# Kernel optimization log

Measured on AMD Instinct MI355X. Metric: run time of the kernel, lower is better.

## Reference

```python
import jax, jax.numpy as jnp
import numpy as np

B, T, C = 4, 2048, 1024
H = 16
D = C // H  # head_dim = 64


def setup_inputs() -> dict:
    key = jax.random.key(0)
    ks = jax.random.split(key, 9)
    s = 1.0 / np.sqrt(C)
    return {
        "x": jax.random.normal(ks[0], (B, T, C), dtype=jnp.float32),
        "Wk": jax.random.uniform(ks[1], (C, C), jnp.float32, -s, s),
        "bk": jax.random.uniform(ks[2], (C,), jnp.float32, -s, s),
        "Wq": jax.random.uniform(ks[3], (C, C), jnp.float32, -s, s),
        "bq": jax.random.uniform(ks[4], (C,), jnp.float32, -s, s),
        "Wv": jax.random.uniform(ks[5], (C, C), jnp.float32, -s, s),
        "bv": jax.random.uniform(ks[6], (C,), jnp.float32, -s, s),
        "Wp": jax.random.uniform(ks[7], (C, C), jnp.float32, -s, s),
        "bp": jax.random.uniform(ks[8], (C,), jnp.float32, -s, s),
    }


def reference(x, Wk, bk, Wq, bq, Wv, bv, Wp, bp):
    # projections -> (B, H, T, D)
    def split_heads(y):
        return y.reshape(B, T, H, D).transpose(0, 2, 1, 3)

    k = split_heads(x @ Wk.T + bk)
    q = split_heads(x @ Wq.T + bq)
    v = split_heads(x @ Wv.T + bv)

    att = jnp.einsum("bhtd,bhsd->bhts", q, k) / np.sqrt(D).astype(np.float32)
    causal = jnp.tril(jnp.ones((T, T), dtype=bool))
    att = jnp.where(causal, att, -jnp.inf)
    att = jax.nn.softmax(att, axis=-1)

    y = jnp.einsum("bhts,bhsd->bhtd", att, v)  # (B,H,T,D)
    y = y.transpose(0, 2, 1, 3).reshape(B, T, C)
    return y @ Wp.T + bp
```

## Files before the change

kernel.cpp:

```cpp
#include <hip/hip_runtime.h>
#include <hip/hip_bf16.h>

typedef unsigned short u16;
typedef unsigned int u32;
typedef short short8 __attribute__((ext_vector_type(8)));
typedef short short4v __attribute__((ext_vector_type(4)));
typedef float f32x4 __attribute__((ext_vector_type(4)));
typedef unsigned int u32x4 __attribute__((ext_vector_type(4)));

#define MFMA16(a, b, c) __builtin_amdgcn_mfma_f32_16x16x32_bf16((a), (b), (c), 0, 0, 0)

constexpr int kB = 4, kT = 2048, kC = 1024, kH = 16, kD = 64;
constexpr int kBT = kB * kT;
constexpr long kQKV = (long)kB * kH * kT * kD;
constexpr float kSC = 0.125f * 1.4426950408889634f;

__device__ inline u16 f2bf(float f) {
    __hip_bfloat16 h = __float2bfloat16(f);
    return *reinterpret_cast<u16*>(&h);
}
__device__ inline u32 pkbf_trunc(float lo, float hi) {
    return __builtin_amdgcn_perm(__builtin_bit_cast(u32, hi),
                                 __builtin_bit_cast(u32, lo), 0x07060302u);
}
__device__ inline u32 pkbf_rne(float lo, float hi) {
    return ((u32)f2bf(hi) << 16) | (u32)f2bf(lo);
}

__device__ inline void cp16(const u16* g, u16* l) {
    __builtin_amdgcn_global_load_lds(
        (const __attribute__((address_space(1))) unsigned int*)g,
        (__attribute__((address_space(3))) unsigned int*)l, 16, 0, 0);
}

__global__ __launch_bounds__(256) void cast_kernel(
    const float* __restrict__ x,  const float* __restrict__ Wk,
    const float* __restrict__ Wq, const float* __restrict__ Wv,
    const float* __restrict__ Wp,
    u16* __restrict__ xb, u16* __restrict__ wkb, u16* __restrict__ wqb,
    u16* __restrict__ wvb, u16* __restrict__ wpb)
{
    const long id = (long)blockIdx.x * 256 + threadIdx.x;
    const float* src;
    u16* dst;
    long off;
    if (id < 2097152) {
        src = x; dst = xb; off = id;
    } else {
        const long w = (id - 2097152) >> 18;
        off = (id - 2097152) & 262143;
        src = (w == 0) ? Wk : (w == 1) ? Wq : (w == 2) ? Wv : Wp;
        dst = (w == 0) ? wkb : (w == 1) ? wqb : (w == 2) ? wvb : wpb;
    }
    f32x4 v = *(const f32x4*)&src[off * 4];
    short4v s = {(short)f2bf(v[0]), (short)f2bf(v[1]),
                 (short)f2bf(v[2]), (short)f2bf(v[3])};
    *(short4v*)&dst[off * 4] = s;
}


__global__ __launch_bounds__(512, 4) void qkv_gemm_bf16(
    const u16* __restrict__ xb, const u16* __restrict__ wall,
    const float* __restrict__ bk, const float* __restrict__ bq,
    const float* __restrict__ bv,
    u16* __restrict__ kw, u16* __restrict__ qw, u16* __restrict__ vw)
{
    __shared__ __align__(16) u16 A2[2][128 * 64];
    __shared__ __align__(16) u16 B2[2][128 * 64];

    const int tid = threadIdx.x;
    const int lane = tid & 63;
    const int wid = tid >> 6;
    const int l15 = lane & 15;
    const int quad = lane >> 4;
    const int wr = wid & 1;
    const int wc = wid >> 1;
    const int m0 = blockIdx.x * 128;
    const int n0c = blockIdx.y * 128;

    f32x4 zero = {0.f, 0.f, 0.f, 0.f};
    f32x4 acc[4][2];
#pragma unroll
    for (int i = 0; i < 4; ++i)
#pragma unroll
        for (int j = 0; j < 2; ++j) acc[i][j] = zero;

    const u16* aS[2]; const u16* bS[2];
    int sD[2];
#pragma unroll
    for (int q = 0; q < 2; ++q) {
        const int slot = q * 512 + tid;
        const int row = slot >> 3, ch = slot & 7;
        aS[q] = xb + (long)(m0 + row) * kC + ((ch ^ (row & 7)) * 8);
        bS[q] = wall + (long)(n0c + row) * kC + ((ch ^ (row & 7)) * 8);
        sD[q] = row * 64 + ch * 8;
    }

    auto stage = [&](int buf, int t) {
        const long ko = (long)t * 64;
#pragma unroll
        for (int q = 0; q < 2; ++q) {
            cp16(aS[q] + ko, &A2[buf][sD[q]]);
            cp16(bS[q] + ko, &B2[buf][sD[q]]);
        }
    };

    int aOff[4][2], bOff[2][2];
#pragma unroll
    for (int i = 0; i < 4; ++i) {
        const int row = wr * 64 + i * 16 + l15;
#pragma unroll
        for (int k2 = 0; k2 < 2; ++k2)
            aOff[i][k2] = row * 64 + (((k2 * 4 + quad) ^ (row & 7)) * 8);
    }
#pragma unroll
    for (int j = 0; j < 2; ++j) {
        const int row = wc * 32 + j * 16 + l15;
#pragma unroll
        for (int k2 = 0; k2 < 2; ++k2)
            bOff[j][k2] = row * 64 + (((k2 * 4 + quad) ^ (row & 7)) * 8);
    }

    stage(0, 0);
    stage(1, 1);
    __syncthreads();

    for (int t = 0; t < 16; ++t) {
        const int c = t & 1;
        const u16* Ab = A2[c];
        const u16* Bb = B2[c];

        short8 am[4][2], bn[2][2];
#pragma unroll
        for (int i = 0; i < 4; ++i)
#pragma unroll
            for (int k2 = 0; k2 < 2; ++k2)
                am[i][k2] = *(const short8*)&Ab[aOff[i][k2]];
#pragma unroll
        for (int j = 0; j < 2; ++j)
#pragma unroll
            for (int k2 = 0; k2 < 2; ++k2)
                bn[j][k2] = *(const short8*)&Bb[bOff[j][k2]];

        __builtin_amdgcn_s_setprio(1);
#pragma unroll
        for (int i = 0; i < 4; ++i)
#pragma unroll
            for (int j = 0; j < 2; ++j) {
                acc[i][j] = MFMA16(am[i][0], bn[j][0], acc[i][j]);
                acc[i][j] = MFMA16(am[i][1], bn[j][1], acc[i][j]);
            }
        __builtin_amdgcn_s_setprio(0);

        if (t + 1 < 16) {
            __syncthreads();
            if (t + 2 < 16) stage(c, t + 2);
        }
    }

    const int z = (n0c >> 10);
    const float scale = (z == 1) ? kSC : 1.0f;
    const float* bias = (z == 0) ? bk : (z == 1) ? bq : bv;
#pragma unroll
    for (int j = 0; j < 2; ++j) {
        const int n = n0c + wc * 32 + j * 16 + l15;
        const int np = n & 1023;
        const float bias_f = bias[np];
        const int h = np >> 6, d = np & 63;
#pragma unroll
        for (int i = 0; i < 4; ++i) {
#pragma unroll
            for (int r = 0; r < 4; ++r) {
                const int m = m0 + wr * 64 + i * 16 + quad * 4 + r;
                const int b = m >> 11, tt = m & 2047;
                const float v = (acc[i][j][r] + bias_f) * scale;
                const int bh = b * kH + h;
                if (z == 2) {
                    vw[((long)bh * kD + d) * kT + tt] = f2bf(v);
                } else {
                    u16* dst = (z == 0) ? kw : qw;
                    dst[((long)bh * kT + tt) * kD + d] = f2bf(v);
                }
            }
        }
    }
}

__global__ __launch_bounds__(256) void qkv_gemm_kernel(
    const float* __restrict__ x,
    const float* __restrict__ Wk, const float* __restrict__ bk,
    const float* __restrict__ Wq, const float* __restrict__ bq,
    const float* __restrict__ Wv, const float* __restrict__ bv,
    u16* __restrict__ kw, u16* __restrict__ qw, u16* __restrict__ vw)
{
    __shared__ u16 As[128 * 32];
    __shared__ u16 Bs[128 * 32];
    const int tid = threadIdx.x;
    const int lane = tid & 63;
    const int wid = tid >> 6;
    const int l15 = lane & 15;
    const int quad = lane >> 4;
    const int m0 = blockIdx.x * 128;
    const int n0 = blockIdx.y * 128;
    const int z = blockIdx.z;

    const float* W = (z == 0) ? Wk : (z == 1) ? Wq : Wv;
    const float* bias = (z == 0) ? bk : (z == 1) ? bq : bv;

    f32x4 zero = {0.f, 0.f, 0.f, 0.f};
    f32x4 acc[4][4];
#pragma unroll
    for (int i = 0; i < 4; ++i)
#pragma unroll
        for (int j = 0; j < 4; ++j) acc[i][j] = zero;

    const int wm = (wid & 1) * 64;
    const int wn = (wid >> 1) * 64;
    const int row4 = tid >> 3;
    const int col4 = (tid & 7) * 4;

    for (int k0 = 0; k0 < kC; k0 += 32) {
#pragma unroll
        for (int p = 0; p < 4; ++p) {
            const int r = p * 32 + row4;
            f32x4 xa = *(const f32x4*)&x[(long)(m0 + r) * kC + k0 + col4];
            f32x4 wa = *(const f32x4*)&W[(long)(n0 + r) * kC + k0 + col4];
            short4v xs = {(short)f2bf(xa[0]), (short)f2bf(xa[1]),
                          (short)f2bf(xa[2]), (short)f2bf(xa[3])};
            short4v wsv = {(short)f2bf(wa[0]), (short)f2bf(wa[1]),
                           (short)f2bf(wa[2]), (short)f2bf(wa[3])};
            *(short4v*)&As[r * 32 + col4] = xs;
            *(short4v*)&Bs[r * 32 + col4] = wsv;
        }
        __syncthreads();
        short8 af[4], bfr[4];
#pragma unroll
        for (int mt = 0; mt < 4; ++mt)
            af[mt] = *(const short8*)&As[(wm + mt * 16 + l15) * 32 + quad * 8];
#pragma unroll
        for (int nt = 0; nt < 4; ++nt)
            bfr[nt] = *(const short8*)&Bs[(wn + nt * 16 + l15) * 32 + quad * 8];
#pragma unroll
        for (int mt = 0; mt < 4; ++mt)
#pragma unroll
            for (int nt = 0; nt < 4; ++nt)
                acc[mt][nt] = MFMA16(af[mt], bfr[nt], acc[mt][nt]);
        __syncthreads();
    }

    const float scale = (z == 1) ? kSC : 1.0f;
#pragma unroll
    for (int nt = 0; nt < 4; ++nt) {
        const int n = n0 + wn + nt * 16 + l15;
        const float bias_f = bias[n];
        const int h = n >> 6, d = n & 63;
#pragma unroll
        for (int mt = 0; mt < 4; ++mt) {
#pragma unroll
            for (int r = 0; r < 4; ++r) {
                const int m = m0 + wm + mt * 16 + quad * 4 + r;
                const int b = m >> 11, t = m & 2047;
                const float v = (acc[mt][nt][r] + bias_f) * scale;
                const int bh = b * kH + h;
                if (z == 2) {
                    vw[((long)bh * kD + d) * kT + t] = f2bf(v);
                } else {
                    u16* dst = (z == 0) ? kw : qw;
                    dst[((long)bh * kT + t) * kD + d] = f2bf(v);
                }
            }
        }
    }
}

__global__ __launch_bounds__(256, 4) void attn_kernel(
    const u16* qw, const u16* kw, const u16* vw, u16* ow)
{
    __shared__ u16 Ks[2][64 * 64];
    __shared__ u16 VT[2][64 * 64];

    const int tid = threadIdx.x;
    const int lane = tid & 63;
    const int wid = tid >> 6;
    const int l15 = lane & 15;
    const int quad = lane >> 4;
    const int id = blockIdx.x;
    const int bh = id & 63;
    constexpr int pperm[16] = {15, 14, 13, 12, 0, 1, 2, 3,
                               11, 10, 9, 8, 4, 5, 6, 7};
    const int p = pperm[id >> 6];
    const int p2 = 2 * p;
    const int n_st = p2 + 2;
    const int tw = p * 128 + wid * 32;

    const float NEG = -1.0e30f;
    f32x4 zero = {0.f, 0.f, 0.f, 0.f};
    const short8 onesf = {(short)0x3F80, (short)0x3F80, (short)0x3F80, (short)0x3F80,
                          (short)0x3F80, (short)0x3F80, (short)0x3F80, (short)0x3F80};

    const int rl7 = l15 & 7;

    const u16* kbase = kw + (long)bh * kT * kD;
    const u16* vbase = vw + (long)bh * kD * kT;

    const u16* kp[2];
    const u16* vp[2];
    int sdst[2];
#pragma unroll
    for (int q = 0; q < 2; ++q) {
        const int slot = q * 256 + tid;
        const int row = slot >> 3;
        const int c = slot & 7;
        const int off = (c ^ (row & 7)) * 8;
        kp[q] = kbase + (long)row * kD + off;
        vp[q] = vbase + (long)row * kT + off;
        sdst[q] = slot * 8;
    }

    auto stage = [&](int buf, int st) {
        u16* kd = Ks[buf];
        u16* vd = VT[buf];
#pragma unroll
        for (int q = 0; q < 2; ++q) {
            cp16(kp[q] + (long)st * (64 * kD), kd + sdst[q]);
            cp16(vp[q] + st * 64,              vd + sdst[q]);
        }
    };

    short8 qf[2][2];
#pragma unroll
    for (int g = 0; g < 2; ++g) {
        const u16* qp = qw + ((long)bh * kT + tw + g * 16 + l15) * kD;
        qf[g][0] = *(const short8*)&qp[quad * 8];
        qf[g][1] = *(const short8*)&qp[32 + quad * 8];
    }

    stage(0, 0);
    stage(1, 1);
    __syncthreads();

    f32x4 oacc[4][2];
#pragma unroll
    for (int mo = 0; mo < 4; ++mo)
#pragma unroll
        for (int g = 0; g < 2; ++g) oacc[mo][g] = zero;
    f32x4 lsum[2] = {zero, zero};

    for (int st = 0; st < n_st; ++st) {
        const int cur = st & 1;
        const u16* K_ = Ks[cur];
        const u16* V_ = VT[cur];

        f32x4 sacc[4][2];
        __builtin_amdgcn_s_setprio(1);
#pragma unroll
        for (int ms = 0; ms < 4; ++ms) {
            const int row = ms * 16 + l15;
            short8 kf0 = *(const short8*)&K_[row * 64 + ((quad ^ rl7) * 8)];
            short8 kf1 = *(const short8*)&K_[row * 64 + (((4 + quad) ^ rl7) * 8)];
#pragma unroll
            for (int g = 0; g < 2; ++g) {
                sacc[ms][g] = MFMA16(kf0, qf[g][0], zero);
                sacc[ms][g] = MFMA16(kf1, qf[g][1], sacc[ms][g]);
            }
        }
        __builtin_amdgcn_s_setprio(0);

        const int dg = st - p2;
        if (dg >= 0) {
#pragma unroll
            for (int g = 0; g < 2; ++g) {
                const int off = wid * 32 + g * 16 + l15 - dg * 64;
#pragma unroll
                for (int ms = 0; ms < 4; ++ms)
#pragma unroll
                    for (int r = 0; r < 4; ++r)
                        if (ms * 16 + quad * 4 + r > off) sacc[ms][g][r] = NEG;
            }
        }

        short8 pfr[2][2];
#pragma unroll
        for (int g = 0; g < 2; ++g) {
#pragma unroll
            for (int k2 = 0; k2 < 2; ++k2) {
                const int msA = k2 * 2, msB = k2 * 2 + 1;
                const float a0 = exp2f(sacc[msA][g][0]);
                const float a1 = exp2f(sacc[msA][g][1]);
                const float a2 = exp2f(sacc[msA][g][2]);
                const float a3 = exp2f(sacc[msA][g][3]);
                const float b0 = exp2f(sacc[msB][g][0]);
                const float b1 = exp2f(sacc[msB][g][1]);
                const float b2 = exp2f(sacc[msB][g][2]);
                const float b3 = exp2f(sacc[msB][g][3]);
                const u32 LA = pkbf_trunc(a0, a1), HA = pkbf_trunc(a2, a3);
                const u32 LB = pkbf_trunc(b0, b1), HB = pkbf_trunc(b2, b3);
                auto pL = __builtin_amdgcn_permlane32_swap(LA, LB, false, false);
                auto pH = __builtin_amdgcn_permlane32_swap(HA, HB, false, false);
                auto rL = __builtin_amdgcn_permlane16_swap(pL[0], pL[1], false, false);
                auto rH = __builtin_amdgcn_permlane16_swap(pH[0], pH[1], false, false);
                u32x4 w;
                w[0] = rL[0]; w[1] = rH[0]; w[2] = rL[1]; w[3] = rH[1];
                pfr[g][k2] = __builtin_bit_cast(short8, w);
            }
        }

#pragma unroll
        for (int g = 0; g < 2; ++g) {
            lsum[g] = MFMA16(onesf, pfr[g][0], lsum[g]);
            lsum[g] = MFMA16(onesf, pfr[g][1], lsum[g]);
        }

        __builtin_amdgcn_s_setprio(1);
#pragma unroll
        for (int mo = 0; mo < 4; ++mo) {
            const int row = mo * 16 + l15;
            short8 vf0 = *(const short8*)&V_[row * 64 + ((quad ^ rl7) * 8)];
            short8 vf1 = *(const short8*)&V_[row * 64 + (((4 + quad) ^ rl7) * 8)];
#pragma unroll
            for (int g = 0; g < 2; ++g) {
                oacc[mo][g] = MFMA16(vf0, pfr[g][0], oacc[mo][g]);
                oacc[mo][g] = MFMA16(vf1, pfr[g][1], oacc[mo][g]);
            }
        }
        __builtin_amdgcn_s_setprio(0);

        if (st + 1 < n_st) {
            __syncthreads();
            if (st + 2 < n_st) stage(cur, st + 2);
        }
    }

#pragma unroll
    for (int g = 0; g < 2; ++g) {
        const float inv = 1.0f / lsum[g][0];
        const int t = tw + g * 16 + l15;
        u16* op = ow + ((long)bh * kT + t) * kD;
#pragma unroll
        for (int mo = 0; mo < 4; ++mo) {
            uint2 ov;
            ov.x = pkbf_rne(oacc[mo][g][0] * inv, oacc[mo][g][1] * inv);
            ov.y = pkbf_rne(oacc[mo][g][2] * inv, oacc[mo][g][3] * inv);
            *(uint2*)&op[mo * 16 + quad * 4] = ov;
        }
    }
}

__global__ __launch_bounds__(512, 4) void out_gemm_bf16(
    const u16* __restrict__ ob, const u16* __restrict__ wpb,
    const float* __restrict__ bp, float* __restrict__ out)
{
    __shared__ __align__(16) u16 A2[2][128 * 64];
    __shared__ __align__(16) u16 B2[2][128 * 64];

    const int tid = threadIdx.x;
    const int lane = tid & 63;
    const int wid = tid >> 6;
    const int l15 = lane & 15;
    const int quad = lane >> 4;
    const int wr = wid & 1;
    const int wc = wid >> 1;
    const int m0 = blockIdx.x * 128;
    const int n0 = blockIdx.y * 128;

    f32x4 zero = {0.f, 0.f, 0.f, 0.f};
    f32x4 acc[4][2];
#pragma unroll
    for (int i = 0; i < 4; ++i)
#pragma unroll
        for (int j = 0; j < 2; ++j) acc[i][j] = zero;

    const u16* aS[2]; const u16* bS[2];
    int sD[2];
#pragma unroll
    for (int q = 0; q < 2; ++q) {
        const int slot = q * 512 + tid;
        const int row = slot >> 3, ch = slot & 7;
        const int m = m0 + row, b = m >> 11, trow = m & 2047;
        aS[q] = ob + (((long)b * kH) * kT + trow) * kD + ((ch ^ (row & 7)) * 8);
        bS[q] = wpb + (long)(n0 + row) * kC + ((ch ^ (row & 7)) * 8);
        sD[q] = row * 64 + ch * 8;
    }

    auto stage = [&](int buf, int t) {
        const long koA = (long)t * kT * kD;
        const long koB = (long)t * 64;
#pragma unroll
        for (int q = 0; q < 2; ++q) {
            cp16(aS[q] + koA, &A2[buf][sD[q]]);
            cp16(bS[q] + koB, &B2[buf][sD[q]]);
        }
    };

    int aOff[4][2], bOff[2][2];
#pragma unroll
    for (int i = 0; i < 4; ++i) {
        const int row = wr * 64 + i * 16 + l15;
#pragma unroll
        for (int k2 = 0; k2 < 2; ++k2)
            aOff[i][k2] = row * 64 + (((k2 * 4 + quad) ^ (row & 7)) * 8);
    }
#pragma unroll
    for (int j = 0; j < 2; ++j) {
        const int row = wc * 32 + j * 16 + l15;
#pragma unroll
        for (int k2 = 0; k2 < 2; ++k2)
            bOff[j][k2] = row * 64 + (((k2 * 4 + quad) ^ (row & 7)) * 8);
    }

    stage(0, 0);
    stage(1, 1);
    __syncthreads();

    for (int t = 0; t < 16; ++t) {
        const int c = t & 1;
        const u16* Ab = A2[c];
        const u16* Bb = B2[c];

        short8 am[4][2], bn[2][2];
#pragma unroll
        for (int i = 0; i < 4; ++i)
#pragma unroll
            for (int k2 = 0; k2 < 2; ++k2)
                am[i][k2] = *(const short8*)&Ab[aOff[i][k2]];
#pragma unroll
        for (int j = 0; j < 2; ++j)
#pragma unroll
            for (int k2 = 0; k2 < 2; ++k2)
                bn[j][k2] = *(const short8*)&Bb[bOff[j][k2]];

        __builtin_amdgcn_s_setprio(1);
#pragma unroll
        for (int i = 0; i < 4; ++i)
#pragma unroll
            for (int j = 0; j < 2; ++j) {
                acc[i][j] = MFMA16(am[i][0], bn[j][0], acc[i][j]);
                acc[i][j] = MFMA16(am[i][1], bn[j][1], acc[i][j]);
            }
        __builtin_amdgcn_s_setprio(0);

        if (t + 1 < 16) {
            __syncthreads();
            if (t + 2 < 16) stage(c, t + 2);
        }
    }

#pragma unroll
    for (int j = 0; j < 2; ++j) {
        const int n = n0 + wc * 32 + j * 16 + l15;
        const float bias_f = bp[n];
#pragma unroll
        for (int i = 0; i < 4; ++i) {
#pragma unroll
            for (int r = 0; r < 4; ++r) {
                const int m = m0 + wr * 64 + i * 16 + quad * 4 + r;
                out[(long)m * kC + n] = acc[i][j][r] + bias_f;
            }
        }
    }
}

__global__ __launch_bounds__(256) void out_gemm_kernel(
    const u16* __restrict__ ow, const float* __restrict__ Wp,
    const float* __restrict__ bp, float* __restrict__ out)
{
    __shared__ u16 As[128 * 32];
    __shared__ u16 Bs[128 * 32];
    const int tid = threadIdx.x;
    const int lane = tid & 63;
    const int wid = tid >> 6;
    const int l15 = lane & 15;
    const int quad = lane >> 4;
    const int m0 = blockIdx.x * 128;
    const int n0 = blockIdx.y * 128;

    f32x4 zero = {0.f, 0.f, 0.f, 0.f};
    f32x4 acc[4][4];
#pragma unroll
    for (int i = 0; i < 4; ++i)
#pragma unroll
        for (int j = 0; j < 4; ++j) acc[i][j] = zero;

    const int wm = (wid & 1) * 64;
    const int wn = (wid >> 1) * 64;

    const int r0 = tid >> 2;
    const int kkA = (tid & 3) * 8;
    const int r1 = r0 + 64;
    const int row4 = tid >> 3;
    const int col4 = (tid & 7) * 4;

    for (int k0 = 0; k0 < kC; k0 += 32) {
        {
            const int m = m0 + r0, b = m >> 11, t = m & 2047;
            const int kk = k0 + kkA, h = kk >> 6, d = kk & 63;
            *(short8*)&As[r0 * 32 + kkA] =
                *(const short8*)&ow[(((long)b * kH + h) * kT + t) * kD + d];
        }
        {
            const int m = m0 + r1, b = m >> 11, t = m & 2047;
            const int kk = k0 + kkA, h = kk >> 6, d = kk & 63;
            *(short8*)&As[r1 * 32 + kkA] =
                *(const short8*)&ow[(((long)b * kH + h) * kT + t) * kD + d];
        }
#pragma unroll
        for (int p = 0; p < 4; ++p) {
            const int r = p * 32 + row4;
            f32x4 wa = *(const f32x4*)&Wp[(long)(n0 + r) * kC + k0 + col4];
            short4v wsv = {(short)f2bf(wa[0]), (short)f2bf(wa[1]),
                           (short)f2bf(wa[2]), (short)f2bf(wa[3])};
            *(short4v*)&Bs[r * 32 + col4] = wsv;
        }
        __syncthreads();
        short8 af[4], bfr[4];
#pragma unroll
        for (int mt = 0; mt < 4; ++mt)
            af[mt] = *(const short8*)&As[(wm + mt * 16 + l15) * 32 + quad * 8];
#pragma unroll
        for (int nt = 0; nt < 4; ++nt)
            bfr[nt] = *(const short8*)&Bs[(wn + nt * 16 + l15) * 32 + quad * 8];
#pragma unroll
        for (int mt = 0; mt < 4; ++mt)
#pragma unroll
            for (int nt = 0; nt < 4; ++nt)
                acc[mt][nt] = MFMA16(af[mt], bfr[nt], acc[mt][nt]);
        __syncthreads();
    }

#pragma unroll
    for (int nt = 0; nt < 4; ++nt) {
        const int n = n0 + wn + nt * 16 + l15;
        const float bias_f = bp[n];
#pragma unroll
        for (int mt = 0; mt < 4; ++mt) {
#pragma unroll
            for (int r = 0; r < 4; ++r) {
                const int m = m0 + wm + mt * 16 + quad * 4 + r;
                out[(long)m * kC + n] = acc[mt][nt][r] + bias_f;
            }
        }
    }
}

extern "C" void kernel_launch(void* const* d_in, const int* in_sizes, int n_in,
                              void* d_out, int out_size, void* d_ws, size_t ws_size,
                              hipStream_t stream) {
    const float* x  = (const float*)d_in[0];
    const float* Wk = (const float*)d_in[1];
    const float* bk = (const float*)d_in[2];
    const float* Wq = (const float*)d_in[3];
    const float* bq = (const float*)d_in[4];
    const float* Wv = (const float*)d_in[5];
    const float* bv = (const float*)d_in[6];
    const float* Wp = (const float*)d_in[7];
    const float* bp = (const float*)d_in[8];
    float* out = (float*)d_out;

    u16* ws = (u16*)d_ws;
    const size_t kNeed = 72ull * 1024 * 1024;

    if (ws_size >= kNeed) {
        u16* k_ws = ws;
        u16* q_ws = ws + kQKV;
        u16* v_ws = ws + 2 * kQKV;
        u16* xb   = ws + 3 * kQKV;
        u16* o_ws = xb;
        u16* wkb  = ws + 4 * kQKV;
        u16* wqb  = wkb + (long)kC * kC;
        u16* wvb  = wqb + (long)kC * kC;
        u16* wpb  = wvb + (long)kC * kC;

        cast_kernel<<<12288, 256, 0, stream>>>(x, Wk, Wq, Wv, Wp,
                                               xb, wkb, wqb, wvb, wpb);
        qkv_gemm_bf16<<<dim3(kBT / 128, 24), 512, 0, stream>>>(
            xb, wkb, bk, bq, bv, k_ws, q_ws, v_ws);
        attn_kernel<<<1024, 256, 0, stream>>>(q_ws, k_ws, v_ws, o_ws);
        out_gemm_bf16<<<dim3(kBT / 128, kC / 128), 512, 0, stream>>>(
            o_ws, wpb, bp, out);
    } else {
        u16* k_ws = ws;
        u16* q_ws = ws + kQKV;
        u16* v_ws = ws + 2 * kQKV;
        u16* o_ws = q_ws;

        qkv_gemm_kernel<<<dim3(kBT / 128, kC / 128, 3), 256, 0, stream>>>(
            x, Wk, bk, Wq, bq, Wv, bv, k_ws, q_ws, v_ws);
        attn_kernel<<<1024, 256, 0, stream>>>(q_ws, k_ws, v_ws, o_ws);
        out_gemm_kernel<<<dim3(kBT / 128, kC / 128), 256, 0, stream>>>(
            o_ws, Wp, bp, out);
    }
}
```

Measured before the change: 246.9 us.

## Widen QKV GEMM tile to 128x256 with single-buffered A and split B MFMA phases

The QKV projection GEMM now computes a 128x256 output tile per block instead of 128x128, so each block's A tile is reused across twice as many columns and the grid halves from 24 to 12 column tiles. A is single-buffered, and B stays double-buffered at twice the size. The next stage is issued right after the A fragments are read into registers, and B fragments are consumed in two halves to keep register pressure down. Each warp now holds twice as many accumulators, which may reduce occupancy, and there is an extra barrier per k-step and fewer blocks to fill the GPU.

```diff
diff --git a/kernel.cpp b/kernel.cpp
--- a/kernel.cpp
+++ b/kernel.cpp
@@ -65,8 +65,8 @@
     const float* __restrict__ bv,
     u16* __restrict__ kw, u16* __restrict__ qw, u16* __restrict__ vw)
 {
-    __shared__ __align__(16) u16 A2[2][128 * 64];
-    __shared__ __align__(16) u16 B2[2][128 * 64];
+    __shared__ __align__(16) u16 As[128 * 64];
+    __shared__ __align__(16) u16 B2[2][256 * 64];
 
     const int tid = threadIdx.x;
     const int lane = tid & 63;
@@ -76,36 +76,41 @@
     const int wr = wid & 1;
     const int wc = wid >> 1;
     const int m0 = blockIdx.x * 128;
-    const int n0c = blockIdx.y * 128;
+    const int n0c = blockIdx.y * 256;
 
     f32x4 zero = {0.f, 0.f, 0.f, 0.f};
-    f32x4 acc[4][2];
+    f32x4 acc[4][4];
 #pragma unroll
     for (int i = 0; i < 4; ++i)
 #pragma unroll
-        for (int j = 0; j < 2; ++j) acc[i][j] = zero;
-
-    const u16* aS[2]; const u16* bS[2];
-    int sD[2];
+        for (int j = 0; j < 4; ++j) acc[i][j] = zero;
+
+    const u16* aS[2]; int aD[2];
 #pragma unroll
     for (int q = 0; q < 2; ++q) {
         const int slot = q * 512 + tid;
         const int row = slot >> 3, ch = slot & 7;
         aS[q] = xb + (long)(m0 + row) * kC + ((ch ^ (row & 7)) * 8);
+        aD[q] = row * 64 + ch * 8;
+    }
+    const u16* bS[4]; int bD[4];
+#pragma unroll
+    for (int q = 0; q < 4; ++q) {
+        const int slot = q * 512 + tid;
+        const int row = slot >> 3, ch = slot & 7;
         bS[q] = wall + (long)(n0c + row) * kC + ((ch ^ (row & 7)) * 8);
-        sD[q] = row * 64 + ch * 8;
-    }
-
-    auto stage = [&](int buf, int t) {
+        bD[q] = row * 64 + ch * 8;
+    }
+
+    auto stage = [&](int t, int bbuf) {
         const long ko = (long)t * 64;
-#pragma unroll
-        for (int q = 0; q < 2; ++q) {
-            cp16(aS[q] + ko, &A2[buf][sD[q]]);
-            cp16(bS[q] + ko, &B2[buf][sD[q]]);
-        }
+        cp16(aS[0] + ko, &As[aD[0]]);
+        cp16(aS[1] + ko, &As[aD[1]]);
+#pragma unroll
+        for (int q = 0; q < 4; ++q) cp16(bS[q] + ko, &B2[bbuf][bD[q]]);
     };
 
-    int aOff[4][2], bOff[2][2];
+    int aOff[4][2], bOff[4][2];
 #pragma unroll
     for (int i = 0; i < 4; ++i) {
         const int row = wr * 64 + i * 16 + l15;
@@ -114,56 +119,73 @@
             aOff[i][k2] = row * 64 + (((k2 * 4 + quad) ^ (row & 7)) * 8);
     }
 #pragma unroll
-    for (int j = 0; j < 2; ++j) {
-        const int row = wc * 32 + j * 16 + l15;
+    for (int j = 0; j < 4; ++j) {
+        const int row = wc * 64 + j * 16 + l15;
 #pragma unroll
         for (int k2 = 0; k2 < 2; ++k2)
             bOff[j][k2] = row * 64 + (((k2 * 4 + quad) ^ (row & 7)) * 8);
     }
 
     stage(0, 0);
-    stage(1, 1);
     __syncthreads();
 
     for (int t = 0; t < 16; ++t) {
         const int c = t & 1;
-        const u16* Ab = A2[c];
         const u16* Bb = B2[c];
 
-        short8 am[4][2], bn[2][2];
+        short8 am[4][2];
 #pragma unroll
         for (int i = 0; i < 4; ++i)
 #pragma unroll
             for (int k2 = 0; k2 < 2; ++k2)
-                am[i][k2] = *(const short8*)&Ab[aOff[i][k2]];
-#pragma unroll
-        for (int j = 0; j < 2; ++j)
-#pragma unroll
-            for (int k2 = 0; k2 < 2; ++k2)
-                bn[j][k2] = *(const short8*)&Bb[bOff[j][k2]];
-
-        __builtin_amdgcn_s_setprio(1);
-#pragma unroll
-        for (int i = 0; i < 4; ++i)
-#pragma unroll
-            for (int j = 0; j < 2; ++j) {
-                acc[i][j] = MFMA16(am[i][0], bn[j][0], acc[i][j]);
-                acc[i][j] = MFMA16(am[i][1], bn[j][1], acc[i][j]);
-            }
-        __builtin_amdgcn_s_setprio(0);
+                am[i][k2] = *(const short8*)&As[aOff[i][k2]];
 
         if (t + 1 < 16) {
             __syncthreads();
-            if (t + 2 < 16) stage(c, t + 2);
-        }
+            stage(t + 1, c ^ 1);
+        }
+
+        short8 bnL[2][2];
+#pragma unroll
+        for (int j = 0; j < 2; ++j)
+#pragma unroll
+            for (int k2 = 0; k2 < 2; ++k2)
+                bnL[j][k2] = *(const short8*)&Bb[bOff[j][k2]];
+        __builtin_amdgcn_s_setprio(1);
+#pragma unroll
+        for (int i = 0; i < 4; ++i)
+#pragma unroll
+            for (int j = 0; j < 2; ++j) {
+                acc[i][j] = MFMA16(am[i][0], bnL[j][0], acc[i][j]);
+                acc[i][j] = MFMA16(am[i][1], bnL[j][1], acc[i][j]);
+            }
+        __builtin_amdgcn_s_setprio(0);
+
+        short8 bnH[2][2];
+#pragma unroll
+        for (int j = 0; j < 2; ++j)
+#pragma unroll
+            for (int k2 = 0; k2 < 2; ++k2)
+                bnH[j][k2] = *(const short8*)&Bb[bOff[2 + j][k2]];
+        __builtin_amdgcn_s_setprio(1);
+#pragma unroll
+        for (int i = 0; i < 4; ++i)
+#pragma unroll
+            for (int j = 0; j < 2; ++j) {
+                acc[i][2 + j] = MFMA16(am[i][0], bnH[j][0], acc[i][2 + j]);
+                acc[i][2 + j] = MFMA16(am[i][1], bnH[j][1], acc[i][2 + j]);
+            }
+        __builtin_amdgcn_s_setprio(0);
+
+        if (t + 1 < 16) __syncthreads();
     }
 
     const int z = (n0c >> 10);
     const float scale = (z == 1) ? kSC : 1.0f;
     const float* bias = (z == 0) ? bk : (z == 1) ? bq : bv;
 #pragma unroll
-    for (int j = 0; j < 2; ++j) {
-        const int n = n0c + wc * 32 + j * 16 + l15;
+    for (int j = 0; j < 4; ++j) {
+        const int n = n0c + wc * 64 + j * 16 + l15;
         const int np = n & 1023;
         const float bias_f = bias[np];
         const int h = np >> 6, d = np & 63;
@@ -672,7 +694,7 @@
 
         cast_kernel<<<12288, 256, 0, stream>>>(x, Wk, Wq, Wv, Wp,
                                                xb, wkb, wqb, wvb, wpb);
-        qkv_gemm_bf16<<<dim3(kBT / 128, 24), 512, 0, stream>>>(
+        qkv_gemm_bf16<<<dim3(kBT / 128, 12), 512, 0, stream>>>(
             xb, wkb, bk, bq, bv, k_ws, q_ws, v_ws);
         attn_kernel<<<1024, 256, 0, stream>>>(q_ws, k_ws, v_ws, o_ws);
         out_gemm_bf16<<<dim3(kBT / 128, kC / 128), 512, 0, stream>>>(
```

New measurement: 295.2 us. 19.5% more time.
